# Kernel optimization log

Hardware: AMD Instinct MI355X
Metric: run time of the kernel (lower is better)

Reference implementation:

```python
import jax, jax.numpy as jnp
import numpy as np

N_NODES = 50000
N_EDGES = 800000


def _sage(x, src, dst, Wl, bl, Wr):
    # mean-aggregate neighbor features (messages flow src -> dst), then linear
    msg = x[src]                                              # [E, d_in]
    s = jax.ops.segment_sum(msg, dst, num_segments=N_NODES)   # [N, d_in]
    cnt = jax.ops.segment_sum(jnp.ones((src.shape[0],), x.dtype), dst,
                              num_segments=N_NODES)           # [N]
    agg = s / jnp.maximum(cnt, 1.0)[:, None]
    return agg @ Wl.T + bl + x @ Wr.T


def setup_inputs() -> dict:
    key = jax.random.key(0)
    ks = jax.random.split(key, 10)
    d_in, h = 128, 64
    def w(k, o, i):
        return jax.random.normal(k, (o, i), jnp.float32) * (1.0 / np.sqrt(i))
    return {
        "x": jax.random.normal(ks[0], (N_NODES, d_in), jnp.float32),
        "edge_index": jax.random.randint(ks[1], (2, N_EDGES), 0, N_NODES, jnp.int64),
        "Wl1": w(ks[2], h, d_in), "bl1": jnp.zeros((h,), jnp.float32), "Wr1": w(ks[3], h, d_in),
        "Wl2": w(ks[4], 2 * h, h), "bl2": jnp.zeros((2 * h,), jnp.float32), "Wr2": w(ks[5], 2 * h, h),
        "Wl3": w(ks[6], 2 * h, 2 * h), "bl3": jnp.zeros((2 * h,), jnp.float32), "Wr3": w(ks[7], 2 * h, 2 * h),
        "Wl4": w(ks[8], h, 2 * h), "bl4": jnp.zeros((h,), jnp.float32), "Wr4": w(ks[9], h, 2 * h),
    }


def reference(x, edge_index, Wl1, bl1, Wr1, Wl2, bl2, Wr2, Wl3, bl3, Wr3, Wl4, bl4, Wr4):
    src, dst = edge_index[0], edge_index[1]
    h = jax.nn.relu(_sage(x, src, dst, Wl1, bl1, Wr1))
    h = jax.nn.relu(_sage(h, src, dst, Wl2, bl2, Wr2))
    h = jax.nn.relu(_sage(h, src, dst, Wl3, bl3, Wr3))
    h = _sage(h, src, dst, Wl4, bl4, Wr4)
    return h
```

## Files before the change

### kernel.cpp

```cpp
#include <hip/hip_runtime.h>

#define NN 50000
#define NE 800000
#define SCB 196
#define GB 391

typedef __attribute__((ext_vector_type(8))) short short8v;
typedef __attribute__((ext_vector_type(4))) float float4v;

__device__ __forceinline__ int uni(int v) { return __builtin_amdgcn_readfirstlane(v); }
__device__ __forceinline__ unsigned short f2bf(float f) {
    unsigned u = __float_as_uint(f);
    return (unsigned short)((u + 0x7FFFu + ((u >> 16) & 1u)) >> 16);
}
__device__ __forceinline__ float bf2f(unsigned short h) {
    return __uint_as_float(((unsigned)h) << 16);
}

__global__ void count_kernel(const int* __restrict__ dst, int* __restrict__ cnt) {
    int i = blockIdx.x * blockDim.x + threadIdx.x;
    if (i < NE) atomicAdd(&cnt[dst[i]], 1);
}

__global__ __launch_bounds__(256) void scan1_kernel(const int* __restrict__ cnt,
                                                    int* __restrict__ part) {
    __shared__ int red[256];
    const int t = threadIdx.x;
    const int i = blockIdx.x * 256 + t;
    red[t] = (i < NN) ? cnt[i] : 0;
    __syncthreads();
#pragma unroll
    for (int d = 128; d > 0; d >>= 1) {
        if (t < d) red[t] += red[t + d];
        __syncthreads();
    }
    if (t == 0) part[blockIdx.x] = red[0];
}

__global__ __launch_bounds__(256) void scan2_kernel(int* __restrict__ part) {
    __shared__ int ps[256];
    const int t = threadIdx.x;
    ps[t] = (t < SCB) ? part[t] : 0;
    __syncthreads();
#pragma unroll
    for (int d = 1; d < 256; d <<= 1) {
        int v = (t >= d) ? ps[t - d] : 0;
        __syncthreads();
        ps[t] += v;
        __syncthreads();
    }
    if (t < SCB) part[t] = (t == 0) ? 0 : ps[t - 1];
}

__global__ __launch_bounds__(256) void scan3_kernel(const int* __restrict__ cnt,
                                                    const int* __restrict__ part,
                                                    int* __restrict__ off,
                                                    int* __restrict__ cursor,
                                                    float* __restrict__ inv) {
    __shared__ int ps[256];
    const int t = threadIdx.x;
    const int i = blockIdx.x * 256 + t;
    const int c = (i < NN) ? cnt[i] : 0;
    ps[t] = c;
    __syncthreads();
#pragma unroll
    for (int d = 1; d < 256; d <<= 1) {
        int v = (t >= d) ? ps[t - d] : 0;
        __syncthreads();
        ps[t] += v;
        __syncthreads();
    }
    if (i < NN) {
        const int o = part[blockIdx.x] + ps[t] - c;
        off[i] = o;
        cursor[i] = o;
        inv[i] = 1.0f / (float)max(c, 1);
    }
}

__global__ void fill_kernel(const int* __restrict__ src, const int* __restrict__ dst,
                            int* __restrict__ cursor, int* __restrict__ srcs) {
    int e = blockIdx.x * blockDim.x + threadIdx.x;
    if (e < NE) {
        int p = atomicAdd(&cursor[dst[e]], 1);
        srcs[p] = src[e];
    }
}

template<int D, int MODE, int SRCBF, int DUALB>
__global__ __launch_bounds__(256) void gather_kernel(
    const void* __restrict__ yv, int ys, const int* __restrict__ srcs,
    const int* __restrict__ off, const int* __restrict__ cnt,
    const float* __restrict__ inv, const float* __restrict__ pre, int ps,
    float* __restrict__ out, int os, unsigned short* __restrict__ outb) {
    const int w = (blockIdx.x * blockDim.x + threadIdx.x) >> 6;
    const int lane = threadIdx.x & 63;
    if (w >= NN) return;
    const int o = uni(off[w]);
    const int n = uni(cnt[w]);
    const float* yf = (const float*)yv;
    const unsigned short* yb = (const unsigned short*)yv;
    float a0 = 0.0f, a1 = 0.0f;
    int i = 0;
    for (; i + 4 <= n; i += 4) {
        int sv[4];
#pragma unroll
        for (int u = 0; u < 4; ++u) sv[u] = srcs[o + i + u];
#pragma unroll
        for (int u = 0; u < 4; ++u) {
            if constexpr (SRCBF) {
                if constexpr (D == 64) {
                    a0 += bf2f(yb[(size_t)sv[u] * ys + lane]);
                } else {
                    const ushort2 v = *reinterpret_cast<const ushort2*>(
                        &yb[(size_t)sv[u] * ys + 2 * lane]);
                    a0 += bf2f(v.x);
                    a1 += bf2f(v.y);
                }
            } else {
                a0 += yf[(size_t)sv[u] * ys + lane];
                if constexpr (D == 128) a1 += yf[(size_t)sv[u] * ys + 64 + lane];
            }
        }
    }
    for (; i < n; ++i) {
        int s = srcs[o + i];
        if constexpr (SRCBF) {
            if constexpr (D == 64) {
                a0 += bf2f(yb[(size_t)s * ys + lane]);
            } else {
                const ushort2 v = *reinterpret_cast<const ushort2*>(
                    &yb[(size_t)s * ys + 2 * lane]);
                a0 += bf2f(v.x);
                a1 += bf2f(v.y);
            }
        } else {
            a0 += yf[(size_t)s * ys + lane];
            if constexpr (D == 128) a1 += yf[(size_t)s * ys + 64 + lane];
        }
    }
    const float iv = inv[w];
    if constexpr (D == 128 && SRCBF) {
        float r0 = a0 * iv, r1 = a1 * iv;
        if constexpr (MODE != 0) {
            const float2 pv = *reinterpret_cast<const float2*>(&pre[(size_t)w * ps + 2 * lane]);
            r0 += pv.x; r1 += pv.y;
        }
        if constexpr (MODE == 1) { r0 = fmaxf(r0, 0.0f); r1 = fmaxf(r1, 0.0f); }
        float2 sv = {r0, r1};
        *reinterpret_cast<float2*>(&out[(size_t)w * os + 2 * lane]) = sv;
    } else {
        float r0 = a0 * iv;
        if constexpr (MODE != 0) r0 += pre[(size_t)w * ps + lane];
        if constexpr (MODE == 1) r0 = fmaxf(r0, 0.0f);
        out[(size_t)w * os + lane] = r0;
        if constexpr (DUALB) outb[(size_t)w * 64 + lane] = f2bf(r0);
        if constexpr (D == 128 && !SRCBF) {
            float r1 = a1 * iv;
            if constexpr (MODE != 0) r1 += pre[(size_t)w * ps + 64 + lane];
            if constexpr (MODE == 1) r1 = fmaxf(r1, 0.0f);
            out[(size_t)w * os + 64 + lane] = r1;
        }
    }
}

struct WSrc { const float* p[8]; };

__global__ __launch_bounds__(256) void wplanes_kernel(WSrc S,
                                                      unsigned short* __restrict__ ph,
                                                      unsigned short* __restrict__ pl) {
    const int e = blockIdx.x * 256 + threadIdx.x;
    const int seg = blockIdx.y;
    const int row = e >> 7, k = e & 127;
    float x;
    switch (seg) {
        case 0:  x = (row < 64) ? S.p[0][row * 128 + k] : S.p[1][(row - 64) * 128 + k]; break;
        case 1:  x = (k < 64)   ? S.p[2][row * 64 + k]  : S.p[3][row * 64 + (k - 64)];  break;
        case 2:  x = S.p[4][e]; break;
        case 3:  x = S.p[5][e]; break;
        default: x = (row < 64) ? S.p[6][row * 128 + k] : S.p[7][(row - 64) * 128 + k]; break;
    }
    const unsigned u = __float_as_uint(x);
    const float lo = x - __uint_as_float(u & 0xFFFF0000u);
    const int o = seg * 16384 + e;
    ph[o] = (unsigned short)(u >> 16);
    pl[o] = (unsigned short)(__float_as_uint(lo) >> 16);
}

__global__ __launch_bounds__(256) void gemm_mfma(
    const float* __restrict__ in,
    const unsigned short* __restrict__ Bh, const unsigned short* __restrict__ Bl,
    float* __restrict__ out0, const float* __restrict__ bias0, int os0, int obf0,
    float* __restrict__ out1, const float* __restrict__ bias1, int os1, int obf1,
    int relu) {
    const int t = threadIdx.x;
    const int lane = t & 63;
    const int wid = t >> 6;
    const int wn = wid & 1;
    const int wc = wid >> 1;
    const int l15 = lane & 15;
    const int lk = lane >> 4;
    const int nb = (int)blockIdx.x * 128 + wn * 64;

    float* const outp = wc ? out1 : out0;
    const float* const biasp = wc ? bias1 : bias0;
    const int os = wc ? os1 : os0;
    const int obf = wc ? obf1 : obf0;
    const unsigned short* const Bhp = Bh + (size_t)(wc * 64) * 128;
    const unsigned short* const Blp = Bl + (size_t)(wc * 64) * 128;
    const ptrdiff_t dlo = Blp - Bhp;

    float4v acc[4][4];
#pragma unroll
    for (int mi = 0; mi < 4; ++mi)
#pragma unroll
        for (int ci = 0; ci < 4; ++ci) acc[mi][ci] = (float4v)0.0f;

    const float* arow[4];
#pragma unroll
    for (int mi = 0; mi < 4; ++mi) {
        int r = nb + mi * 16 + l15;
        if (r > NN - 1) r = NN - 1;
        arow[mi] = in + (size_t)r * 128;
    }
    const unsigned short* brow[4];
#pragma unroll
    for (int ci = 0; ci < 4; ++ci) brow[ci] = Bhp + (size_t)(ci * 16 + l15) * 128;

    for (int ks = 0; ks < 4; ++ks) {
        const int ko = ks * 32 + lk * 8;
        short8v Ah[4], Al[4];
#pragma unroll
        for (int mi = 0; mi < 4; ++mi) {
            const float4v v0 = *reinterpret_cast<const float4v*>(arow[mi] + ko);
            const float4v v1 = *reinterpret_cast<const float4v*>(arow[mi] + ko + 4);
            float xv[8] = {v0.x, v0.y, v0.z, v0.w, v1.x, v1.y, v1.z, v1.w};
            union { unsigned u[4]; short8v s; } H, L;
#pragma unroll
            for (int q = 0; q < 4; ++q) {
                const unsigned u0 = __float_as_uint(xv[2 * q]);
                const unsigned u1 = __float_as_uint(xv[2 * q + 1]);
                const float l0 = xv[2 * q]     - __uint_as_float(u0 & 0xFFFF0000u);
                const float l1 = xv[2 * q + 1] - __uint_as_float(u1 & 0xFFFF0000u);
                H.u[q] = (u1 & 0xFFFF0000u) | (u0 >> 16);
                L.u[q] = (__float_as_uint(l1) & 0xFFFF0000u) | (__float_as_uint(l0) >> 16);
            }
            Ah[mi] = H.s;
            Al[mi] = L.s;
        }
        short8v Bhf[4], Blf[4];
#pragma unroll
        for (int ci = 0; ci < 4; ++ci) {
            Bhf[ci] = *reinterpret_cast<const short8v*>(brow[ci] + ko);
            Blf[ci] = *reinterpret_cast<const short8v*>(brow[ci] + dlo + ko);
        }
#pragma unroll
        for (int mi = 0; mi < 4; ++mi)
#pragma unroll
            for (int ci = 0; ci < 4; ++ci) {
                acc[mi][ci] = __builtin_amdgcn_mfma_f32_16x16x32_bf16(Ah[mi], Bhf[ci], acc[mi][ci], 0, 0, 0);
                acc[mi][ci] = __builtin_amdgcn_mfma_f32_16x16x32_bf16(Ah[mi], Blf[ci], acc[mi][ci], 0, 0, 0);
                acc[mi][ci] = __builtin_amdgcn_mfma_f32_16x16x32_bf16(Al[mi], Bhf[ci], acc[mi][ci], 0, 0, 0);
            }
    }

#pragma unroll
    for (int ci = 0; ci < 4; ++ci) {
        const int c = ci * 16 + l15;
        const float b = biasp ? biasp[c] : 0.0f;
#pragma unroll
        for (int mi = 0; mi < 4; ++mi) {
#pragma unroll
            for (int j = 0; j < 4; ++j) {
                const int r = nb + mi * 16 + lk * 4 + j;
                if (r < NN) {
                    float v = acc[mi][ci][j] + b;
                    if (relu) v = fmaxf(v, 0.0f);
                    if (obf) ((unsigned short*)outp)[(size_t)r * os + c] = f2bf(v);
                    else outp[(size_t)r * os + c] = v;
                }
            }
        }
    }
}

extern "C" void kernel_launch(void* const* d_in, const int* in_sizes, int n_in,
                              void* d_out, int out_size, void* d_ws, size_t ws_size,
                              hipStream_t stream) {
    const float* x   = (const float*)d_in[0];
    const int*   eix = (const int*)d_in[1];
    const float* Wl1 = (const float*)d_in[2];
    const float* bl1 = (const float*)d_in[3];
    const float* Wr1 = (const float*)d_in[4];
    const float* Wl2 = (const float*)d_in[5];
    const float* bl2 = (const float*)d_in[6];
    const float* Wr2 = (const float*)d_in[7];
    const float* Wl3 = (const float*)d_in[8];
    const float* bl3 = (const float*)d_in[9];
    const float* Wr3 = (const float*)d_in[10];
    const float* Wl4 = (const float*)d_in[11];
    const float* bl4 = (const float*)d_in[12];
    const float* Wr4 = (const float*)d_in[13];
    float* out = (float*)d_out;

    const int* src = eix;
    const int* dst = eix + NE;

    char* ws = (char*)d_ws;
    int*   cnt    = (int*)ws;
    int*   off    = cnt + NN;
    int*   cursor = off + NN;
    float* inv    = (float*)(cursor + NN);
    int*   part   = (int*)(inv + NN);
    int*   srcs   = part + 256;
    unsigned short* ph = (unsigned short*)(srcs + NE);
    unsigned short* pl = ph + 81920;
    unsigned short* XB1 = pl + 81920;
    unsigned short* H1B = XB1 + (size_t)NN * 64;
    unsigned short* G3B = XB1;
    float* HCAT = (float*)(XB1 + (size_t)NN * 128);
    float* H2   = HCAT + (size_t)NN * 128;
    float* HPRE = H2 + (size_t)NN * 128;

    hipMemsetAsync(cnt, 0, NN * sizeof(int), stream);
    count_kernel<<<(NE + 255) / 256, 256, 0, stream>>>(dst, cnt);
    scan1_kernel<<<SCB, 256, 0, stream>>>(cnt, part);
    scan2_kernel<<<1, 256, 0, stream>>>(part);
    scan3_kernel<<<SCB, 256, 0, stream>>>(cnt, part, off, cursor, inv);
    fill_kernel<<<(NE + 255) / 256, 256, 0, stream>>>(src, dst, cursor, srcs);

    {
        WSrc s;
        s.p[0] = Wl1; s.p[1] = Wr1; s.p[2] = Wl2; s.p[3] = Wr2;
        s.p[4] = Wl3; s.p[5] = Wr3; s.p[6] = Wl4; s.p[7] = Wr4;
        wplanes_kernel<<<dim3(64, 5), 256, 0, stream>>>(s, ph, pl);
    }

    gemm_mfma<<<GB, 256, 0, stream>>>(x, ph, pl,
                                      (float*)XB1, nullptr, 64, 1,
                                      HCAT + 64, bl1, 128, 0, 0);
    gather_kernel<64, 1, 1, 1><<<12500, 256, 0, stream>>>(
        XB1, 64, srcs, off, cnt, inv, HCAT + 64, 128, HCAT + 64, 128, H1B);

    gather_kernel<64, 0, 1, 0><<<12500, 256, 0, stream>>>(
        H1B, 64, srcs, off, cnt, inv, nullptr, 0, HCAT, 128, nullptr);
    gemm_mfma<<<GB, 256, 0, stream>>>(HCAT, ph + 16384, pl + 16384,
                                      H2, bl2, 128, 0,
                                      H2 + 64, bl2 + 64, 128, 0, 1);

    gemm_mfma<<<GB, 256, 0, stream>>>(H2, ph + 2 * 16384, pl + 2 * 16384,
                                      (float*)G3B, nullptr, 128, 1,
                                      (float*)(G3B + 64), nullptr, 128, 1, 0);
    gemm_mfma<<<GB, 256, 0, stream>>>(H2, ph + 3 * 16384, pl + 3 * 16384,
                                      HPRE, bl3, 128, 0,
                                      HPRE + 64, bl3 + 64, 128, 0, 0);
    gather_kernel<128, 1, 1, 0><<<12500, 256, 0, stream>>>(
        G3B, 128, srcs, off, cnt, inv, HPRE, 128, HPRE, 128, nullptr);

    gemm_mfma<<<GB, 256, 0, stream>>>(HPRE, ph + 4 * 16384, pl + 4 * 16384,
                                      HCAT, nullptr, 64, 0,
                                      out, bl4, 64, 0, 0);
    gather_kernel<64, 2, 0, 0><<<12500, 256, 0, stream>>>(
        HCAT, 64, srcs, off, cnt, inv, out, 64, out, 64, nullptr);
}
```

Before: 369.6 us.

## Build CSR via two-level bucket sort with LDS atomics; bf16 last-layer gather

Replaces the global-atomic count/scan/fill CSR construction with a histogram over 256-node buckets, a scan, a partition pass, and a per-bucket finalize that does local counting and placement using shared-memory atomics. Source and low destination bits are packed into one word, with the scratch buffer borrowed from an unused activation buffer. The final layer's GEMM output is also stored as bf16 so the last gather reads half the bytes. This adds more kernel launches and relies on node ids fitting in 16 bits, and the bf16 storage adds rounding error to the last layer.

New measurement: 324.6 us. 1.14x faster.

```diff
diff --git a/kernel.cpp b/kernel.cpp
--- a/kernel.cpp
+++ b/kernel.cpp
@@ -2,8 +2,12 @@
 
 #define NN 50000
 #define NE 800000
-#define SCB 196
 #define GB 391
+#define NBUK 196
+#define PB 128
+#define CH 6250
+#define HLEN (NBUK * PB)
+#define SAB (HLEN / 256)
 
 typedef __attribute__((ext_vector_type(8))) short short8v;
 typedef __attribute__((ext_vector_type(4))) float float4v;
@@ -17,17 +21,27 @@
     return __uint_as_float(((unsigned)h) << 16);
 }
 
-__global__ void count_kernel(const int* __restrict__ dst, int* __restrict__ cnt) {
-    int i = blockIdx.x * blockDim.x + threadIdx.x;
-    if (i < NE) atomicAdd(&cnt[dst[i]], 1);
-}
-
-__global__ __launch_bounds__(256) void scan1_kernel(const int* __restrict__ cnt,
+__global__ __launch_bounds__(256) void hist_kernel(const int* __restrict__ dst,
+                                                   int* __restrict__ H) {
+    __shared__ int h[NBUK];
+    const int t = threadIdx.x;
+    const int b = blockIdx.x;
+    if (t < NBUK) h[t] = 0;
+    __syncthreads();
+    const int e0 = b * CH;
+    for (int i = t; i < CH; i += 256) {
+        int e = e0 + i;
+        if (e < NE) atomicAdd(&h[dst[e] >> 8], 1);
+    }
+    __syncthreads();
+    if (t < NBUK) H[t * PB + b] = h[t];
+}
+
+__global__ __launch_bounds__(256) void scanA_kernel(const int* __restrict__ a,
                                                     int* __restrict__ part) {
     __shared__ int red[256];
     const int t = threadIdx.x;
-    const int i = blockIdx.x * 256 + t;
-    red[t] = (i < NN) ? cnt[i] : 0;
+    red[t] = a[blockIdx.x * 256 + t];
     __syncthreads();
 #pragma unroll
     for (int d = 128; d > 0; d >>= 1) {
@@ -37,10 +51,28 @@
     if (t == 0) part[blockIdx.x] = red[0];
 }
 
-__global__ __launch_bounds__(256) void scan2_kernel(int* __restrict__ part) {
+__global__ __launch_bounds__(128) void scanB_kernel(int* __restrict__ part) {
+    __shared__ int ps[128];
+    const int t = threadIdx.x;
+    ps[t] = (t < SAB) ? part[t] : 0;
+    __syncthreads();
+#pragma unroll
+    for (int d = 1; d < 128; d <<= 1) {
+        int v = (t >= d) ? ps[t - d] : 0;
+        __syncthreads();
+        ps[t] += v;
+        __syncthreads();
+    }
+    if (t < SAB) part[t] = (t == 0) ? 0 : ps[t - 1];
+}
+
+__global__ __launch_bounds__(256) void scanC_kernel(int* __restrict__ a,
+                                                    const int* __restrict__ part) {
     __shared__ int ps[256];
     const int t = threadIdx.x;
-    ps[t] = (t < SCB) ? part[t] : 0;
+    const int i = blockIdx.x * 256 + t;
+    const int c = a[i];
+    ps[t] = c;
     __syncthreads();
 #pragma unroll
     for (int d = 1; d < 256; d <<= 1) {
@@ -49,18 +81,51 @@
         ps[t] += v;
         __syncthreads();
     }
-    if (t < SCB) part[t] = (t == 0) ? 0 : ps[t - 1];
-}
-
-__global__ __launch_bounds__(256) void scan3_kernel(const int* __restrict__ cnt,
-                                                    const int* __restrict__ part,
-                                                    int* __restrict__ off,
-                                                    int* __restrict__ cursor,
-                                                    float* __restrict__ inv) {
+    a[i] = part[blockIdx.x] + ps[t] - c;
+}
+
+__global__ __launch_bounds__(256) void partition_kernel(const int* __restrict__ src,
+                                                        const int* __restrict__ dst,
+                                                        const int* __restrict__ Hs,
+                                                        unsigned* __restrict__ tmp) {
+    __shared__ int cur[NBUK];
+    const int t = threadIdx.x;
+    const int b = blockIdx.x;
+    if (t < NBUK) cur[t] = Hs[t * PB + b];
+    __syncthreads();
+    const int e0 = b * CH;
+    for (int i = t; i < CH; i += 256) {
+        int e = e0 + i;
+        if (e < NE) {
+            const int d = dst[e];
+            const int k = d >> 8;
+            const int pos = atomicAdd(&cur[k], 1);
+            tmp[pos] = (unsigned)src[e] | ((unsigned)(d & 255) << 16);
+        }
+    }
+}
+
+__global__ __launch_bounds__(256) void finalize_kernel(const unsigned* __restrict__ tmp,
+                                                       const int* __restrict__ Hs,
+                                                       int* __restrict__ off,
+                                                       int* __restrict__ cnt,
+                                                       float* __restrict__ inv,
+                                                       int* __restrict__ srcs) {
+    __shared__ int hist[256];
     __shared__ int ps[256];
-    const int t = threadIdx.x;
-    const int i = blockIdx.x * 256 + t;
-    const int c = (i < NN) ? cnt[i] : 0;
+    __shared__ int cur[256];
+    const int t = threadIdx.x;
+    const int k = blockIdx.x;
+    const int s0 = Hs[k * PB];
+    const int end = (k == NBUK - 1) ? NE : Hs[(k + 1) * PB];
+    const int m = end - s0;
+    hist[t] = 0;
+    __syncthreads();
+    for (int i = t; i < m; i += 256) {
+        atomicAdd(&hist[(tmp[s0 + i] >> 16) & 255], 1);
+    }
+    __syncthreads();
+    const int c = hist[t];
     ps[t] = c;
     __syncthreads();
 #pragma unroll
@@ -70,20 +135,19 @@
         ps[t] += v;
         __syncthreads();
     }
-    if (i < NN) {
-        const int o = part[blockIdx.x] + ps[t] - c;
-        off[i] = o;
-        cursor[i] = o;
-        inv[i] = 1.0f / (float)max(c, 1);
-    }
-}
-
-__global__ void fill_kernel(const int* __restrict__ src, const int* __restrict__ dst,
-                            int* __restrict__ cursor, int* __restrict__ srcs) {
-    int e = blockIdx.x * blockDim.x + threadIdx.x;
-    if (e < NE) {
-        int p = atomicAdd(&cursor[dst[e]], 1);
-        srcs[p] = src[e];
+    const int ex = ps[t] - c;
+    const int node = k * 256 + t;
+    if (node < NN) {
+        off[node] = s0 + ex;
+        cnt[node] = c;
+        inv[node] = 1.0f / (float)max(c, 1);
+    }
+    cur[t] = s0 + ex;
+    __syncthreads();
+    for (int i = t; i < m; i += 256) {
+        const unsigned u = tmp[s0 + i];
+        const int p = atomicAdd(&cur[(u >> 16) & 255], 1);
+        srcs[p] = (int)(u & 0xFFFFu);
     }
 }
 
@@ -307,12 +371,12 @@
     const int* dst = eix + NE;
 
     char* ws = (char*)d_ws;
-    int*   cnt    = (int*)ws;
-    int*   off    = cnt + NN;
-    int*   cursor = off + NN;
-    float* inv    = (float*)(cursor + NN);
-    int*   part   = (int*)(inv + NN);
-    int*   srcs   = part + 256;
+    int*   cnt  = (int*)ws;
+    int*   off  = cnt + NN;
+    float* inv  = (float*)(off + NN);
+    int*   Hs   = (int*)(inv + NN);
+    int*   part = Hs + HLEN;
+    int*   srcs = part + 256;
     unsigned short* ph = (unsigned short*)(srcs + NE);
     unsigned short* pl = ph + 81920;
     unsigned short* XB1 = pl + 81920;
@@ -321,13 +385,15 @@
     float* HCAT = (float*)(XB1 + (size_t)NN * 128);
     float* H2   = HCAT + (size_t)NN * 128;
     float* HPRE = H2 + (size_t)NN * 128;
-
-    hipMemsetAsync(cnt, 0, NN * sizeof(int), stream);
-    count_kernel<<<(NE + 255) / 256, 256, 0, stream>>>(dst, cnt);
-    scan1_kernel<<<SCB, 256, 0, stream>>>(cnt, part);
-    scan2_kernel<<<1, 256, 0, stream>>>(part);
-    scan3_kernel<<<SCB, 256, 0, stream>>>(cnt, part, off, cursor, inv);
-    fill_kernel<<<(NE + 255) / 256, 256, 0, stream>>>(src, dst, cursor, srcs);
+    unsigned*       tmp = (unsigned*)HPRE;
+    unsigned short* G4B = (unsigned short*)HCAT;
+
+    hist_kernel<<<PB, 256, 0, stream>>>(dst, Hs);
+    scanA_kernel<<<SAB, 256, 0, stream>>>(Hs, part);
+    scanB_kernel<<<1, 128, 0, stream>>>(part);
+    scanC_kernel<<<SAB, 256, 0, stream>>>(Hs, part);
+    partition_kernel<<<PB, 256, 0, stream>>>(src, dst, Hs, tmp);
+    finalize_kernel<<<NBUK, 256, 0, stream>>>(tmp, Hs, off, cnt, inv, srcs);
 
     {
         WSrc s;
@@ -358,8 +424,8 @@
         G3B, 128, srcs, off, cnt, inv, HPRE, 128, HPRE, 128, nullptr);
 
     gemm_mfma<<<GB, 256, 0, stream>>>(HPRE, ph + 4 * 16384, pl + 4 * 16384,
-                                      HCAT, nullptr, 64, 0,
+                                      (float*)G4B, nullptr, 64, 1,
                                       out, bl4, 64, 0, 0);
-    gather_kernel<64, 2, 0, 0><<<12500, 256, 0, stream>>>(
-        HCAT, 64, srcs, off, cnt, inv, out, 64, out, 64, nullptr);
-}
+    gather_kernel<64, 2, 1, 0><<<12500, 256, 0, stream>>>(
+        G4B, 64, srcs, off, cnt, inv, out, 64, out, 64, nullptr);
+}
```
